# Kernel optimization log

Measured on AMD Instinct MI355X. Metric: run time of the kernel, lower is better.

## Reference

```python
import jax, jax.numpy as jnp
import numpy as np

HOPS = 4
ALPHA = 0.1
N = 100000   # nodes
E = 1600000  # edges (before self loops)
DX = 128     # x feature dim
DY = 32      # y (soft label) dim


def setup_inputs() -> dict:
    key = jax.random.key(0)
    k1, k2, k3, k4 = jax.random.split(key, 4)
    x = jax.random.normal(k1, (N, DX), dtype=jnp.float32)
    y = jax.random.normal(k2, (N, DY), dtype=jnp.float32)
    src = jax.random.randint(k3, (E,), 0, N)
    dst = jax.random.randint(k4, (E,), 0, N)
    # emulate remove_self_loops with static shapes: perturb any accidental self loop
    dst = jnp.where(src == dst, (dst + 1) % N, dst)
    edge_index = jnp.stack([src, dst]).astype(jnp.int64)
    return {"x": x, "y": y, "edge_index": edge_index}


def reference(x, y, edge_index):
    src, dst = edge_index[0], edge_index[1]
    # add_self_loops (edge_index already has self loops removed)
    loop = jnp.arange(N, dtype=src.dtype)
    src = jnp.concatenate([src, loop])
    dst = jnp.concatenate([dst, loop])
    # symmetric normalization: w_e = deg(src)^-1/2 * deg(dst)^-1/2, deg counted on dst
    deg = jax.ops.segment_sum(jnp.ones_like(dst, dtype=x.dtype), dst, num_segments=N)
    dinv = jnp.where(deg > 0, deg ** -0.5, 0.0)
    w = dinv[src] * dinv[dst]  # [E+N]

    def spmm(v):
        # adj[src, dst] = w  =>  (adj @ v)[i] = sum_{e: src_e = i} w_e * v[dst_e]
        return jax.ops.segment_sum(w[:, None] * v[dst], src, num_segments=N)

    for _ in range(HOPS):
        x_prime = spmm(x)
        y_prime = spmm(y)
        if ALPHA > 0:
            x_prime = (1.0 - ALPHA) * x_prime + ALPHA * x
            y_prime = (1.0 - ALPHA) * y_prime + ALPHA * y
        x, y = x_prime, y_prime
    return x, y
```

## Files before the change

### kernel.cpp

```cpp
#include <hip/hip_runtime.h>


#define NN 100000
#define EE 1600000
#define NPAD 100096
#define NBKT 391
#define CHUNK 4096
#define CAP2 5120

#define GETREG_XCC_IMM (((32 - 1) << 11) | (0 << 6) | 20)

__device__ __forceinline__ float bflo(unsigned w) { return __uint_as_float(w << 16); }
__device__ __forceinline__ float bfhi(unsigned w) { return __uint_as_float(w & 0xffff0000u); }
__device__ __forceinline__ unsigned packbf(float a, float b) {
    unsigned ua = __float_as_uint(a), ub = __float_as_uint(b);
    unsigned ra = (ua + 0x7fffu + ((ua >> 16) & 1u)) >> 16;
    unsigned rb = (ub + 0x7fffu + ((ub >> 16) & 1u)) >> 16;
    return ra | (rb << 16);
}


__global__ void detect_kernel(const int* __restrict__ raw, int* __restrict__ flag) {
    if (threadIdx.x == 0 && blockIdx.x == 0) {
        int is64 = 1;
        for (int k = 1; k < 16; k += 2) {
            if (raw[k] != 0) { is64 = 0; break; }
        }
        *flag = is64;
    }
}

__global__ void zero_kernel(int* __restrict__ bufs, int total) {
    int i = blockIdx.x * blockDim.x + threadIdx.x;
    if (i < total) bufs[i] = 0;
}

__global__ __launch_bounds__(256) void passA_kernel(const void* __restrict__ raw,
                                                    const int* __restrict__ flag,
                                                    int* __restrict__ indeg_rep,
                                                    int* __restrict__ gbcur,
                                                    int* __restrict__ buf) {
    __shared__ unsigned short sh_b[CHUNK];
    __shared__ unsigned int   sh_p[CHUNK];
    __shared__ unsigned int   sh_sorted[CHUNK];
    __shared__ unsigned short sh_bs[CHUNK];
    __shared__ int hist[512];
    __shared__ int excl[512];
    __shared__ int gbase[512];
    __shared__ int lcur[512];

    int tid = threadIdx.x;
    int base = blockIdx.x * CHUNK;
    int nval = EE - base; if (nval > CHUNK) nval = CHUNK;
    int r = __builtin_amdgcn_s_getreg(GETREG_XCC_IMM) & 7;
    int is64 = *flag;

    hist[tid] = 0; hist[tid + 256] = 0;
    __syncthreads();

    for (int i = tid; i < nval; i += 256) {
        int e = base + i;
        int s, d;
        if (is64) {
            s = (int)((const long long*)raw)[e];
            d = (int)((const long long*)raw)[EE + e];
        } else {
            s = ((const int*)raw)[e];
            d = ((const int*)raw)[EE + e];
        }
        atomicAdd(&indeg_rep[r * NPAD + d], 1);
        int b = s >> 8;
        sh_b[i] = (unsigned short)b;
        sh_p[i] = ((unsigned)(s & 255) << 17) | (unsigned)d;
        atomicAdd(&hist[b], 1);
    }
    __syncthreads();

    excl[tid] = hist[tid];
    excl[tid + 256] = hist[tid + 256];
    __syncthreads();
    for (int off = 1; off < 512; off <<= 1) {
        int a0 = (tid >= off) ? excl[tid - off] : 0;
        int a1 = (tid + 256 >= off) ? excl[tid + 256 - off] : 0;
        __syncthreads();
        excl[tid] += a0;
        excl[tid + 256] += a1;
        __syncthreads();
    }
    int inc0 = excl[tid], inc1 = excl[tid + 256];
    int h0 = hist[tid],  h1 = hist[tid + 256];
    __syncthreads();
    int e0 = inc0 - h0, e1 = inc1 - h1;
    excl[tid] = e0; excl[tid + 256] = e1;
    lcur[tid] = e0; lcur[tid + 256] = e1;
    if (h0 > 0) gbase[tid]       = atomicAdd(&gbcur[tid * 16], h0);
    if (h1 > 0) gbase[tid + 256] = atomicAdd(&gbcur[(tid + 256) * 16], h1);
    __syncthreads();

    for (int i = tid; i < nval; i += 256) {
        int b = sh_b[i];
        int pos = atomicAdd(&lcur[b], 1);
        sh_sorted[pos] = sh_p[i];
        sh_bs[pos] = (unsigned short)b;
    }
    __syncthreads();

    for (int i = tid; i < nval; i += 256) {
        int b = sh_bs[i];
        int gpos = gbase[b] + (i - excl[b]);
        if (gpos < CAP2)
            buf[(size_t)b * CAP2 + gpos] = (int)sh_sorted[i];
    }
}

__global__ void bucket_scan_kernel(const int* __restrict__ gbcur, int* __restrict__ bucket_base,
                                   int* __restrict__ rowptr) {
    __shared__ int s[512];
    int tid = threadIdx.x;
    int v = 0;
    if (tid < NBKT) {
        int c = gbcur[tid * 16];
        v = (c < CAP2) ? c : CAP2;
    }
    s[tid] = v;
    __syncthreads();
    for (int off = 1; off < 512; off <<= 1) {
        int t = (tid >= off) ? s[tid - off] : 0;
        __syncthreads();
        s[tid] += t;
        __syncthreads();
    }
    if (tid < NBKT) bucket_base[tid] = s[tid] - v;
    if (tid == 0) rowptr[NN] = EE;
}

__global__ void dinv_kernel(const int* __restrict__ indeg_rep, float* __restrict__ dinv) {
    int i = blockIdx.x * blockDim.x + threadIdx.x;
    if (i < NN) {
        int ind = 1;
        #pragma unroll
        for (int r = 0; r < 8; ++r) ind += indeg_rep[r * NPAD + i];
        dinv[i] = rsqrtf((float)ind);
    }
}

__global__ void cast_kernel(const float4* __restrict__ x0, const float4* __restrict__ y0,
                            const float* __restrict__ dinv, uint4* __restrict__ zx,
                            uint4* __restrict__ zy) {
    int t = blockIdx.x * blockDim.x + threadIdx.x;
    if (t < NN * 16) {
        int node = t >> 4, c = t & 15;
        float di = dinv[node];
        float4 a = x0[(size_t)node * 32 + c * 2];
        float4 b = x0[(size_t)node * 32 + c * 2 + 1];
        uint4 o;
        o.x = packbf(di * a.x, di * a.y); o.y = packbf(di * a.z, di * a.w);
        o.z = packbf(di * b.x, di * b.y); o.w = packbf(di * b.z, di * b.w);
        zx[(size_t)node * 16 + c] = o;
    } else if (t < NN * 20) {
        int u = t - NN * 16;
        int node = u >> 2, c = u & 3;
        float di = dinv[node];
        float4 a = y0[(size_t)node * 8 + c * 2];
        float4 b = y0[(size_t)node * 8 + c * 2 + 1];
        uint4 o;
        o.x = packbf(di * a.x, di * a.y); o.y = packbf(di * a.z, di * a.w);
        o.z = packbf(di * b.x, di * b.y); o.w = packbf(di * b.z, di * b.w);
        zy[(size_t)node * 4 + c] = o;
    }
}

__global__ __launch_bounds__(256) void passB_kernel(const int* __restrict__ gbcur,
                                                    const int* __restrict__ buf,
                                                    const int* __restrict__ bucket_base,
                                                    int* __restrict__ rowptr,
                                                    int* __restrict__ dst_sorted) {
    int b = blockIdx.x;
    int tid = threadIdx.x;
    __shared__ int edges[CAP2];
    __shared__ int hist[256];
    __shared__ int sc[256];
    __shared__ int base_s, tot_s;

    if (tid == 0) {
        int c = gbcur[b * 16];
        tot_s = (c < CAP2) ? c : CAP2;
        base_s = bucket_base[b];
    }
    hist[tid] = 0;
    __syncthreads();
    int total = tot_s;
    const int* src = buf + (size_t)b * CAP2;
    for (int i = tid; i < total; i += 256) {
        int p = src[i];
        edges[i] = p;
        atomicAdd(&hist[p >> 17], 1);
    }
    __syncthreads();
    int hv = hist[tid];
    sc[tid] = hv;
    __syncthreads();
    for (int o = 1; o < 256; o <<= 1) {
        int t = (tid >= o) ? sc[tid - o] : 0;
        __syncthreads();
        sc[tid] += t;
        __syncthreads();
    }
    int excl = sc[tid] - hv;
    int node = (b << 8) + tid;
    if (node < NN) rowptr[node] = base_s + excl;
    hist[tid] = excl;
    __syncthreads();
    for (int i = tid; i < total; i += 256) {
        int p = edges[i];
        int pos = atomicAdd(&hist[p >> 17], 1);
        dst_sorted[base_s + pos] = p & 0x1ffff;
    }
}

template <bool OUTBF>
__global__ __launch_bounds__(256) void hop_kernel(const int* __restrict__ rowptr,
                                                  const int* __restrict__ dst_sorted,
                                                  const float* __restrict__ dinv,
                                                  const uint4* __restrict__ zx,
                                                  const uint4* __restrict__ zy,
                                                  void* __restrict__ nx,
                                                  void* __restrict__ ny) {
    int t = blockIdx.x * blockDim.x + threadIdx.x;
    int row = t >> 6, lane = t & 63;
    if (row >= NN) return;
    int beg = rowptr[row], end = rowptr[row + 1];

    int g = lane >> 4, sub = lane & 15;
    float ax[8] = {0.f, 0.f, 0.f, 0.f, 0.f, 0.f, 0.f, 0.f};
    for (int e = beg + g; e < end; e += 4) {
        int d = dst_sorted[e];
        uint4 w = zx[(size_t)d * 16 + sub];
        ax[0] += bflo(w.x); ax[1] += bfhi(w.x);
        ax[2] += bflo(w.y); ax[3] += bfhi(w.y);
        ax[4] += bflo(w.z); ax[5] += bfhi(w.z);
        ax[6] += bflo(w.w); ax[7] += bfhi(w.w);
    }
    #pragma unroll
    for (int m = 16; m <= 32; m <<= 1) {
        #pragma unroll
        for (int i = 0; i < 8; ++i) ax[i] += __shfl_xor(ax[i], m);
    }

    int gy = lane >> 2, sy = lane & 3;
    float ay[8] = {0.f, 0.f, 0.f, 0.f, 0.f, 0.f, 0.f, 0.f};
    for (int e = beg + gy; e < end; e += 16) {
        int d = dst_sorted[e];
        uint4 w = zy[(size_t)d * 4 + sy];
        ay[0] += bflo(w.x); ay[1] += bfhi(w.x);
        ay[2] += bflo(w.y); ay[3] += bfhi(w.y);
        ay[4] += bflo(w.z); ay[5] += bfhi(w.z);
        ay[6] += bflo(w.w); ay[7] += bfhi(w.w);
    }
    #pragma unroll
    for (int m = 4; m <= 32; m <<= 1) {
        #pragma unroll
        for (int i = 0; i < 8; ++i) ay[i] += __shfl_xor(ay[i], m);
    }

    float di = dinv[row];
    float sg = 0.9f * di;
    float sl = 0.9f * di + 0.1f / di;

    if (g == 0) {
        uint4 wz = zx[(size_t)row * 16 + sub];
        float c[8] = { bflo(wz.x), bfhi(wz.x), bflo(wz.y), bfhi(wz.y),
                       bflo(wz.z), bfhi(wz.z), bflo(wz.w), bfhi(wz.w) };
        float r[8];
        #pragma unroll
        for (int i = 0; i < 8; ++i) r[i] = sg * ax[i] + sl * c[i];
        if constexpr (OUTBF) {
            uint4 o;
            o.x = packbf(di * r[0], di * r[1]); o.y = packbf(di * r[2], di * r[3]);
            o.z = packbf(di * r[4], di * r[5]); o.w = packbf(di * r[6], di * r[7]);
            ((uint4*)nx)[(size_t)row * 16 + sub] = o;
        } else {
            float4 a, b;
            a.x = r[0]; a.y = r[1]; a.z = r[2]; a.w = r[3];
            b.x = r[4]; b.y = r[5]; b.z = r[6]; b.w = r[7];
            ((float4*)nx)[(size_t)row * 32 + sub * 2]     = a;
            ((float4*)nx)[(size_t)row * 32 + sub * 2 + 1] = b;
        }
    }
    if (gy == 0) {
        uint4 wz = zy[(size_t)row * 4 + sy];
        float c[8] = { bflo(wz.x), bfhi(wz.x), bflo(wz.y), bfhi(wz.y),
                       bflo(wz.z), bfhi(wz.z), bflo(wz.w), bfhi(wz.w) };
        float r[8];
        #pragma unroll
        for (int i = 0; i < 8; ++i) r[i] = sg * ay[i] + sl * c[i];
        if constexpr (OUTBF) {
            uint4 o;
            o.x = packbf(di * r[0], di * r[1]); o.y = packbf(di * r[2], di * r[3]);
            o.z = packbf(di * r[4], di * r[5]); o.w = packbf(di * r[6], di * r[7]);
            ((uint4*)ny)[(size_t)row * 4 + sy] = o;
        } else {
            float4 a, b;
            a.x = r[0]; a.y = r[1]; a.z = r[2]; a.w = r[3];
            b.x = r[4]; b.y = r[5]; b.z = r[6]; b.w = r[7];
            ((float4*)ny)[(size_t)row * 8 + sy * 2]     = a;
            ((float4*)ny)[(size_t)row * 8 + sy * 2 + 1] = b;
        }
    }
}

extern "C" void kernel_launch(void* const* d_in, const int* in_sizes, int n_in,
                              void* d_out, int out_size, void* d_ws, size_t ws_size,
                              hipStream_t stream) {
    const float* x0  = (const float*)d_in[0];
    const float* y0  = (const float*)d_in[1];
    const void*  raw = d_in[2];

    float* out_x = (float*)d_out;
    float* out_y = out_x + (size_t)NN * 128;

    int*   flag        = (int*)d_ws;
    int*   indeg_rep   = flag + 16;
    int*   gbcur       = indeg_rep + 8 * NPAD;
    int*   bucket_base = gbcur + 512 * 16;
    int*   rowptr      = bucket_base + 512;
    float* dinv        = (float*)(rowptr + 100112);
    int*   buf         = (int*)(dinv + NPAD);
    int*   dst_sorted  = buf + (size_t)NBKT * CAP2;
    uint4* zxA         = (uint4*)(dst_sorted + EE);
    uint4* zxB         = zxA + (size_t)NN * 16;
    uint4* zyA         = (uint4*)(zxB + (size_t)NN * 16);
    uint4* zyB         = zyA + (size_t)NN * 4;

    const int B = 256;
    const int GW = (NN * 64 + B - 1) / B;
    const int ZTOT = 8 * NPAD + 512 * 16;

    detect_kernel<<<1, 64, 0, stream>>>((const int*)raw, flag);
    zero_kernel<<<(ZTOT + B - 1) / B, B, 0, stream>>>(indeg_rep, ZTOT);
    passA_kernel<<<(EE + CHUNK - 1) / CHUNK, 256, 0, stream>>>(raw, flag, indeg_rep, gbcur, buf);
    bucket_scan_kernel<<<1, 512, 0, stream>>>(gbcur, bucket_base, rowptr);
    dinv_kernel<<<(NN + B - 1) / B, B, 0, stream>>>(indeg_rep, dinv);
    cast_kernel<<<(NN * 20 + B - 1) / B, B, 0, stream>>>(
        (const float4*)x0, (const float4*)y0, dinv, zxA, zyA);
    passB_kernel<<<NBKT, 256, 0, stream>>>(gbcur, buf, bucket_base, rowptr, dst_sorted);

    hop_kernel<true><<<GW, B, 0, stream>>>(rowptr, dst_sorted, dinv, zxA, zyA, zxB, zyB);
    hop_kernel<true><<<GW, B, 0, stream>>>(rowptr, dst_sorted, dinv, zxB, zyB, zxA, zyA);
    hop_kernel<true><<<GW, B, 0, stream>>>(rowptr, dst_sorted, dinv, zxA, zyA, zxB, zyB);
    hop_kernel<false><<<GW, B, 0, stream>>>(rowptr, dst_sorted, dinv, zxB, zyB, out_x, out_y);
}
```

Before: 615.4 us.

## Interleave x/y bf16 features per node and unroll gather loop with masked tails

Stores each node's x and y bf16 features contiguously in one 320-byte record and gathers both in a single fused edge loop. The loop is unrolled to issue up to ten independent gathers per iteration, with clamped indices and multiplicative masks in place of per-edge loop bounds. The detect kernel is folded into the zero kernel to save a launch. This aims to raise memory-level parallelism and reuse the dst index load for both features, at the cost of more registers and some wasted loads on short rows.

```diff
diff --git a/kernel.cpp b/kernel.cpp
--- a/kernel.cpp
+++ b/kernel.cpp
@@ -20,19 +20,17 @@
 }
 
 
-__global__ void detect_kernel(const int* __restrict__ raw, int* __restrict__ flag) {
-    if (threadIdx.x == 0 && blockIdx.x == 0) {
+__global__ void zero_kernel(int* __restrict__ bufs, int total,
+                            const int* __restrict__ raw, int* __restrict__ flag) {
+    int i = blockIdx.x * blockDim.x + threadIdx.x;
+    if (i < total) bufs[i] = 0;
+    if (i == 0) {
         int is64 = 1;
         for (int k = 1; k < 16; k += 2) {
             if (raw[k] != 0) { is64 = 0; break; }
         }
         *flag = is64;
     }
-}
-
-__global__ void zero_kernel(int* __restrict__ bufs, int total) {
-    int i = blockIdx.x * blockDim.x + threadIdx.x;
-    if (i < total) bufs[i] = 0;
 }
 
 __global__ __launch_bounds__(256) void passA_kernel(const void* __restrict__ raw,
@@ -145,8 +143,7 @@
 }
 
 __global__ void cast_kernel(const float4* __restrict__ x0, const float4* __restrict__ y0,
-                            const float* __restrict__ dinv, uint4* __restrict__ zx,
-                            uint4* __restrict__ zy) {
+                            const float* __restrict__ dinv, uint4* __restrict__ zxy) {
     int t = blockIdx.x * blockDim.x + threadIdx.x;
     if (t < NN * 16) {
         int node = t >> 4, c = t & 15;
@@ -156,7 +153,7 @@
         uint4 o;
         o.x = packbf(di * a.x, di * a.y); o.y = packbf(di * a.z, di * a.w);
         o.z = packbf(di * b.x, di * b.y); o.w = packbf(di * b.z, di * b.w);
-        zx[(size_t)node * 16 + c] = o;
+        zxy[(size_t)node * 20 + c] = o;
     } else if (t < NN * 20) {
         int u = t - NN * 16;
         int node = u >> 2, c = u & 3;
@@ -166,7 +163,7 @@
         uint4 o;
         o.x = packbf(di * a.x, di * a.y); o.y = packbf(di * a.z, di * a.w);
         o.z = packbf(di * b.x, di * b.y); o.w = packbf(di * b.z, di * b.w);
-        zy[(size_t)node * 4 + c] = o;
+        zxy[(size_t)node * 20 + 16 + c] = o;
     }
 }
 
@@ -222,53 +219,143 @@
 __global__ __launch_bounds__(256) void hop_kernel(const int* __restrict__ rowptr,
                                                   const int* __restrict__ dst_sorted,
                                                   const float* __restrict__ dinv,
-                                                  const uint4* __restrict__ zx,
-                                                  const uint4* __restrict__ zy,
+                                                  const uint4* __restrict__ z,
                                                   void* __restrict__ nx,
                                                   void* __restrict__ ny) {
     int t = blockIdx.x * blockDim.x + threadIdx.x;
     int row = t >> 6, lane = t & 63;
     if (row >= NN) return;
     int beg = rowptr[row], end = rowptr[row + 1];
+    float di = dinv[row];
 
     int g = lane >> 4, sub = lane & 15;
+    int gy = lane >> 2, sy = lane & 3;
+
     float ax[8] = {0.f, 0.f, 0.f, 0.f, 0.f, 0.f, 0.f, 0.f};
-    for (int e = beg + g; e < end; e += 4) {
-        int d = dst_sorted[e];
-        uint4 w = zx[(size_t)d * 16 + sub];
-        ax[0] += bflo(w.x); ax[1] += bfhi(w.x);
-        ax[2] += bflo(w.y); ax[3] += bfhi(w.y);
-        ax[4] += bflo(w.z); ax[5] += bfhi(w.z);
-        ax[6] += bflo(w.w); ax[7] += bfhi(w.w);
-    }
+    float ay[8] = {0.f, 0.f, 0.f, 0.f, 0.f, 0.f, 0.f, 0.f};
+
+    int last = (end > beg) ? end - 1 : beg;
+
+    for (int e0 = beg; e0 < end; e0 += 32) {
+        int a0 = e0 + g, a1 = e0 + 4 + g, a2 = e0 + 8 + g, a3 = e0 + 12 + g;
+        int aY = e0 + gy;
+        int dA0 = dst_sorted[min(a0, last)];
+        int dA1 = dst_sorted[min(a1, last)];
+        int dA2 = dst_sorted[min(a2, last)];
+        int dA3 = dst_sorted[min(a3, last)];
+        int dAy = dst_sorted[min(aY, last)];
+        uint4 wA0 = z[(size_t)dA0 * 20 + sub];
+        uint4 wA1 = z[(size_t)dA1 * 20 + sub];
+        uint4 wA2 = z[(size_t)dA2 * 20 + sub];
+        uint4 wA3 = z[(size_t)dA3 * 20 + sub];
+        uint4 wAy = z[(size_t)dAy * 20 + 16 + sy];
+        float mA0 = (a0 <= last) ? 1.f : 0.f;
+        float mA1 = (a1 <= last) ? 1.f : 0.f;
+        float mA2 = (a2 <= last) ? 1.f : 0.f;
+        float mA3 = (a3 <= last) ? 1.f : 0.f;
+        float mAy = (aY <= last) ? 1.f : 0.f;
+
+        bool doB = (e0 + 16) < end;
+        if (doB) {
+            int b0 = e0 + 16 + g, b1 = e0 + 20 + g, b2 = e0 + 24 + g, b3 = e0 + 28 + g;
+            int bY = e0 + 16 + gy;
+            int dB0 = dst_sorted[min(b0, last)];
+            int dB1 = dst_sorted[min(b1, last)];
+            int dB2 = dst_sorted[min(b2, last)];
+            int dB3 = dst_sorted[min(b3, last)];
+            int dBy = dst_sorted[min(bY, last)];
+            uint4 wB0 = z[(size_t)dB0 * 20 + sub];
+            uint4 wB1 = z[(size_t)dB1 * 20 + sub];
+            uint4 wB2 = z[(size_t)dB2 * 20 + sub];
+            uint4 wB3 = z[(size_t)dB3 * 20 + sub];
+            uint4 wBy = z[(size_t)dBy * 20 + 16 + sy];
+            float mB0 = (b0 <= last) ? 1.f : 0.f;
+            float mB1 = (b1 <= last) ? 1.f : 0.f;
+            float mB2 = (b2 <= last) ? 1.f : 0.f;
+            float mB3 = (b3 <= last) ? 1.f : 0.f;
+            float mBy = (bY <= last) ? 1.f : 0.f;
+
+            ax[0] += mA0 * bflo(wA0.x); ax[1] += mA0 * bfhi(wA0.x);
+            ax[2] += mA0 * bflo(wA0.y); ax[3] += mA0 * bfhi(wA0.y);
+            ax[4] += mA0 * bflo(wA0.z); ax[5] += mA0 * bfhi(wA0.z);
+            ax[6] += mA0 * bflo(wA0.w); ax[7] += mA0 * bfhi(wA0.w);
+            ax[0] += mA1 * bflo(wA1.x); ax[1] += mA1 * bfhi(wA1.x);
+            ax[2] += mA1 * bflo(wA1.y); ax[3] += mA1 * bfhi(wA1.y);
+            ax[4] += mA1 * bflo(wA1.z); ax[5] += mA1 * bfhi(wA1.z);
+            ax[6] += mA1 * bflo(wA1.w); ax[7] += mA1 * bfhi(wA1.w);
+            ax[0] += mA2 * bflo(wA2.x); ax[1] += mA2 * bfhi(wA2.x);
+            ax[2] += mA2 * bflo(wA2.y); ax[3] += mA2 * bfhi(wA2.y);
+            ax[4] += mA2 * bflo(wA2.z); ax[5] += mA2 * bfhi(wA2.z);
+            ax[6] += mA2 * bflo(wA2.w); ax[7] += mA2 * bfhi(wA2.w);
+            ax[0] += mA3 * bflo(wA3.x); ax[1] += mA3 * bfhi(wA3.x);
+            ax[2] += mA3 * bflo(wA3.y); ax[3] += mA3 * bfhi(wA3.y);
+            ax[4] += mA3 * bflo(wA3.z); ax[5] += mA3 * bfhi(wA3.z);
+            ax[6] += mA3 * bflo(wA3.w); ax[7] += mA3 * bfhi(wA3.w);
+            ay[0] += mAy * bflo(wAy.x); ay[1] += mAy * bfhi(wAy.x);
+            ay[2] += mAy * bflo(wAy.y); ay[3] += mAy * bfhi(wAy.y);
+            ay[4] += mAy * bflo(wAy.z); ay[5] += mAy * bfhi(wAy.z);
+            ay[6] += mAy * bflo(wAy.w); ay[7] += mAy * bfhi(wAy.w);
+
+            ax[0] += mB0 * bflo(wB0.x); ax[1] += mB0 * bfhi(wB0.x);
+            ax[2] += mB0 * bflo(wB0.y); ax[3] += mB0 * bfhi(wB0.y);
+            ax[4] += mB0 * bflo(wB0.z); ax[5] += mB0 * bfhi(wB0.z);
+            ax[6] += mB0 * bflo(wB0.w); ax[7] += mB0 * bfhi(wB0.w);
+            ax[0] += mB1 * bflo(wB1.x); ax[1] += mB1 * bfhi(wB1.x);
+            ax[2] += mB1 * bflo(wB1.y); ax[3] += mB1 * bfhi(wB1.y);
+            ax[4] += mB1 * bflo(wB1.z); ax[5] += mB1 * bfhi(wB1.z);
+            ax[6] += mB1 * bflo(wB1.w); ax[7] += mB1 * bfhi(wB1.w);
+            ax[0] += mB2 * bflo(wB2.x); ax[1] += mB2 * bfhi(wB2.x);
+            ax[2] += mB2 * bflo(wB2.y); ax[3] += mB2 * bfhi(wB2.y);
+            ax[4] += mB2 * bflo(wB2.z); ax[5] += mB2 * bfhi(wB2.z);
+            ax[6] += mB2 * bflo(wB2.w); ax[7] += mB2 * bfhi(wB2.w);
+            ax[0] += mB3 * bflo(wB3.x); ax[1] += mB3 * bfhi(wB3.x);
+            ax[2] += mB3 * bflo(wB3.y); ax[3] += mB3 * bfhi(wB3.y);
+            ax[4] += mB3 * bflo(wB3.z); ax[5] += mB3 * bfhi(wB3.z);
+            ax[6] += mB3 * bflo(wB3.w); ax[7] += mB3 * bfhi(wB3.w);
+            ay[0] += mBy * bflo(wBy.x); ay[1] += mBy * bfhi(wBy.x);
+            ay[2] += mBy * bflo(wBy.y); ay[3] += mBy * bfhi(wBy.y);
+            ay[4] += mBy * bflo(wBy.z); ay[5] += mBy * bfhi(wBy.z);
+            ay[6] += mBy * bflo(wBy.w); ay[7] += mBy * bfhi(wBy.w);
+        } else {
+            ax[0] += mA0 * bflo(wA0.x); ax[1] += mA0 * bfhi(wA0.x);
+            ax[2] += mA0 * bflo(wA0.y); ax[3] += mA0 * bfhi(wA0.y);
+            ax[4] += mA0 * bflo(wA0.z); ax[5] += mA0 * bfhi(wA0.z);
+            ax[6] += mA0 * bflo(wA0.w); ax[7] += mA0 * bfhi(wA0.w);
+            ax[0] += mA1 * bflo(wA1.x); ax[1] += mA1 * bfhi(wA1.x);
+            ax[2] += mA1 * bflo(wA1.y); ax[3] += mA1 * bfhi(wA1.y);
+            ax[4] += mA1 * bflo(wA1.z); ax[5] += mA1 * bfhi(wA1.z);
+            ax[6] += mA1 * bflo(wA1.w); ax[7] += mA1 * bfhi(wA1.w);
+            ax[0] += mA2 * bflo(wA2.x); ax[1] += mA2 * bfhi(wA2.x);
+            ax[2] += mA2 * bflo(wA2.y); ax[3] += mA2 * bfhi(wA2.y);
+            ax[4] += mA2 * bflo(wA2.z); ax[5] += mA2 * bfhi(wA2.z);
+            ax[6] += mA2 * bflo(wA2.w); ax[7] += mA2 * bfhi(wA2.w);
+            ax[0] += mA3 * bflo(wA3.x); ax[1] += mA3 * bfhi(wA3.x);
+            ax[2] += mA3 * bflo(wA3.y); ax[3] += mA3 * bfhi(wA3.y);
+            ax[4] += mA3 * bflo(wA3.z); ax[5] += mA3 * bfhi(wA3.z);
+            ax[6] += mA3 * bflo(wA3.w); ax[7] += mA3 * bfhi(wA3.w);
+            ay[0] += mAy * bflo(wAy.x); ay[1] += mAy * bfhi(wAy.x);
+            ay[2] += mAy * bflo(wAy.y); ay[3] += mAy * bfhi(wAy.y);
+            ay[4] += mAy * bflo(wAy.z); ay[5] += mAy * bfhi(wAy.z);
+            ay[6] += mAy * bflo(wAy.w); ay[7] += mAy * bfhi(wAy.w);
+        }
+    }
+
     #pragma unroll
     for (int m = 16; m <= 32; m <<= 1) {
         #pragma unroll
         for (int i = 0; i < 8; ++i) ax[i] += __shfl_xor(ax[i], m);
     }
-
-    int gy = lane >> 2, sy = lane & 3;
-    float ay[8] = {0.f, 0.f, 0.f, 0.f, 0.f, 0.f, 0.f, 0.f};
-    for (int e = beg + gy; e < end; e += 16) {
-        int d = dst_sorted[e];
-        uint4 w = zy[(size_t)d * 4 + sy];
-        ay[0] += bflo(w.x); ay[1] += bfhi(w.x);
-        ay[2] += bflo(w.y); ay[3] += bfhi(w.y);
-        ay[4] += bflo(w.z); ay[5] += bfhi(w.z);
-        ay[6] += bflo(w.w); ay[7] += bfhi(w.w);
-    }
     #pragma unroll
     for (int m = 4; m <= 32; m <<= 1) {
         #pragma unroll
         for (int i = 0; i < 8; ++i) ay[i] += __shfl_xor(ay[i], m);
     }
 
-    float di = dinv[row];
     float sg = 0.9f * di;
     float sl = 0.9f * di + 0.1f / di;
 
     if (g == 0) {
-        uint4 wz = zx[(size_t)row * 16 + sub];
+        uint4 wz = z[(size_t)row * 20 + sub];
         float c[8] = { bflo(wz.x), bfhi(wz.x), bflo(wz.y), bfhi(wz.y),
                        bflo(wz.z), bfhi(wz.z), bflo(wz.w), bfhi(wz.w) };
         float r[8];
@@ -278,7 +365,7 @@
             uint4 o;
             o.x = packbf(di * r[0], di * r[1]); o.y = packbf(di * r[2], di * r[3]);
             o.z = packbf(di * r[4], di * r[5]); o.w = packbf(di * r[6], di * r[7]);
-            ((uint4*)nx)[(size_t)row * 16 + sub] = o;
+            ((uint4*)nx)[(size_t)row * 20 + sub] = o;
         } else {
             float4 a, b;
             a.x = r[0]; a.y = r[1]; a.z = r[2]; a.w = r[3];
@@ -288,7 +375,7 @@
         }
     }
     if (gy == 0) {
-        uint4 wz = zy[(size_t)row * 4 + sy];
+        uint4 wz = z[(size_t)row * 20 + 16 + sy];
         float c[8] = { bflo(wz.x), bfhi(wz.x), bflo(wz.y), bfhi(wz.y),
                        bflo(wz.z), bfhi(wz.z), bflo(wz.w), bfhi(wz.w) };
         float r[8];
@@ -298,7 +385,7 @@
             uint4 o;
             o.x = packbf(di * r[0], di * r[1]); o.y = packbf(di * r[2], di * r[3]);
             o.z = packbf(di * r[4], di * r[5]); o.w = packbf(di * r[6], di * r[7]);
-            ((uint4*)ny)[(size_t)row * 4 + sy] = o;
+            ((uint4*)nx)[(size_t)row * 20 + 16 + sy] = o;
         } else {
             float4 a, b;
             a.x = r[0]; a.y = r[1]; a.z = r[2]; a.w = r[3];
@@ -327,26 +414,23 @@
     float* dinv        = (float*)(rowptr + 100112);
     int*   buf         = (int*)(dinv + NPAD);
     int*   dst_sorted  = buf + (size_t)NBKT * CAP2;
-    uint4* zxA         = (uint4*)(dst_sorted + EE);
-    uint4* zxB         = zxA + (size_t)NN * 16;
-    uint4* zyA         = (uint4*)(zxB + (size_t)NN * 16);
-    uint4* zyB         = zyA + (size_t)NN * 4;
+    uint4* zxyA        = (uint4*)(dst_sorted + EE);
+    uint4* zxyB        = zxyA + (size_t)NN * 20;
 
     const int B = 256;
     const int GW = (NN * 64 + B - 1) / B;
     const int ZTOT = 8 * NPAD + 512 * 16;
 
-    detect_kernel<<<1, 64, 0, stream>>>((const int*)raw, flag);
-    zero_kernel<<<(ZTOT + B - 1) / B, B, 0, stream>>>(indeg_rep, ZTOT);
+    zero_kernel<<<(ZTOT + B - 1) / B, B, 0, stream>>>(indeg_rep, ZTOT, (const int*)raw, flag);
     passA_kernel<<<(EE + CHUNK - 1) / CHUNK, 256, 0, stream>>>(raw, flag, indeg_rep, gbcur, buf);
     bucket_scan_kernel<<<1, 512, 0, stream>>>(gbcur, bucket_base, rowptr);
     dinv_kernel<<<(NN + B - 1) / B, B, 0, stream>>>(indeg_rep, dinv);
     cast_kernel<<<(NN * 20 + B - 1) / B, B, 0, stream>>>(
-        (const float4*)x0, (const float4*)y0, dinv, zxA, zyA);
+        (const float4*)x0, (const float4*)y0, dinv, zxyA);
     passB_kernel<<<NBKT, 256, 0, stream>>>(gbcur, buf, bucket_base, rowptr, dst_sorted);
 
-    hop_kernel<true><<<GW, B, 0, stream>>>(rowptr, dst_sorted, dinv, zxA, zyA, zxB, zyB);
-    hop_kernel<true><<<GW, B, 0, stream>>>(rowptr, dst_sorted, dinv, zxB, zyB, zxA, zyA);
-    hop_kernel<true><<<GW, B, 0, stream>>>(rowptr, dst_sorted, dinv, zxA, zyA, zxB, zyB);
-    hop_kernel<false><<<GW, B, 0, stream>>>(rowptr, dst_sorted, dinv, zxB, zyB, out_x, out_y);
-}
+    hop_kernel<true><<<GW, B, 0, stream>>>(rowptr, dst_sorted, dinv, zxyA, zxyB, zxyB);
+    hop_kernel<true><<<GW, B, 0, stream>>>(rowptr, dst_sorted, dinv, zxyB, zxyA, zxyA);
+    hop_kernel<true><<<GW, B, 0, stream>>>(rowptr, dst_sorted, dinv, zxyA, zxyB, zxyB);
+    hop_kernel<false><<<GW, B, 0, stream>>>(rowptr, dst_sorted, dinv, zxyB, out_x, out_y);
+}
```

Result: slower. 632.9 us (+2.8%).
